# Optimization experiments

Hardware: AMD Instinct MI355X
Metric: run time of the kernel (lower is better)

The kernel has to match this reference:

```python
import jax, jax.numpy as jnp
import numpy as np

D_MODEL = 4096
N_HEADS = 32
N_KV_HEADS = 32
D_HEAD = 128
D_LATENT = 512
N_CKV = 4            # n_compressed_kv_heads = d_latent // d_head
T = 2048             # num_tokens (single-sequence prefill)
ROPE_BASE = 10000.0
NEG = -1e30


def _rope(x, positions):
    """Neox-style rotary embedding. x: (T, H, D)."""
    d = x.shape[-1]
    inv_freq = 1.0 / (ROPE_BASE ** (jnp.arange(0, d // 2, dtype=jnp.float32) * (2.0 / d)))
    freqs = positions.astype(jnp.float32)[:, None] * inv_freq[None, :]  # (T, D/2)
    cos = jnp.cos(freqs)[:, None, :]
    sin = jnp.sin(freqs)[:, None, :]
    x1, x2 = jnp.split(x, 2, axis=-1)
    return jnp.concatenate([x1 * cos - x2 * sin, x2 * cos + x1 * sin], axis=-1)


def setup_inputs() -> dict:
    key = jax.random.key(0)
    ks = jax.random.split(key, 6)
    s = jnp.float32(0.02)
    return {
        "positions": jnp.arange(T, dtype=jnp.int32),
        "hidden_states": jax.random.normal(ks[0], (T, D_MODEL), jnp.float32),
        "Wq": jax.random.normal(ks[1], (D_MODEL, N_HEADS * D_HEAD), jnp.float32) * s,
        "Wc": jax.random.normal(ks[2], (D_MODEL, 2 * D_LATENT), jnp.float32) * s,
        "Wuk": jax.random.normal(ks[3], (2 * D_LATENT, N_KV_HEADS * D_HEAD), jnp.float32) * s,
        "Wuv": jax.random.normal(ks[4], (2 * D_LATENT, N_KV_HEADS * D_HEAD), jnp.float32) * s,
        "Wo": jax.random.normal(ks[5], (N_HEADS * D_HEAD, D_MODEL), jnp.float32) * s,
    }


def reference(positions, hidden_states, Wq, Wc, Wuk, Wuv, Wo):
    # Q projection
    q = (hidden_states @ Wq).reshape(T, N_HEADS, D_HEAD)
    # MLA compression: hidden -> c_kv (2*d_latent), split into c_k / c_v
    c_kv = hidden_states @ Wc                                   # (T, 2*D_LATENT)
    c_k = c_kv[:, :D_LATENT].reshape(T, N_CKV, D_HEAD)          # compressed K cache
    c_v = c_kv[:, D_LATENT:].reshape(T, N_CKV, D_HEAD)          # compressed V cache
    # Decompression (computed by the source module; K is RoPE'd then discarded,
    # V is unused -- the v1 attention path runs over the compressed cache).
    K = (c_kv @ Wuk).reshape(T, N_KV_HEADS, D_HEAD)
    V = (c_kv @ Wuv).reshape(T, N_KV_HEADS, D_HEAD)             # noqa: unused, matches source
    # RoPE on q (and K, whose rotated value is dead in the source)
    q = _rope(q, positions)
    K = _rope(K, positions)  # dead, kept for FLOP parity with the source
    # GQA attention: n_heads=32 query heads over n_compressed_kv_heads=4 kv heads
    g = N_HEADS // N_CKV
    qg = q.reshape(T, N_CKV, g, D_HEAD)
    scale = jnp.float32(1.0 / np.sqrt(D_HEAD))
    scores = jnp.einsum('tkgd,skd->kgts', qg, c_k) * scale      # (N_CKV, g, T, T)
    causal = positions[:, None] >= positions[None, :]           # (T, T)
    scores = jnp.where(causal[None, None], scores, NEG)
    probs = jax.nn.softmax(scores, axis=-1)
    ctx = jnp.einsum('kgts,skd->tkgd', probs, c_v).reshape(T, N_HEADS * D_HEAD)
    return ctx @ Wo
```

## Files before the change

kernel.cpp:

```cpp
#include <hip/hip_runtime.h>
#include <hip/hip_bf16.h>
#include <cstdint>
#include <cstddef>


typedef unsigned short u16;
typedef short s16x8 __attribute__((ext_vector_type(8)));
typedef short s16x4 __attribute__((ext_vector_type(4)));
typedef float f32x4 __attribute__((ext_vector_type(4)));

#define MFMA16(a, b, c) __builtin_amdgcn_mfma_f32_16x16x32_bf16((a), (b), (c), 0, 0, 0)

#define QSCALE 0.12751899f
#define LOG2_ROPE_BASE 13.287712379549449f
#define FIXMAX 24.0f

__device__ __forceinline__ u16 f2b(float f) {
  return __builtin_bit_cast(u16, __float2bfloat16(f));
}
__device__ __forceinline__ void async_copy16(u16* lds, const u16* g) {
  __builtin_amdgcn_global_load_lds(
      (const __attribute__((address_space(1))) unsigned int*)g,
      (__attribute__((address_space(3))) unsigned int*)lds, 16, 0, 0);
}

__global__ __launch_bounds__(256)
void prep_kernel(const float* __restrict__ hidden, const float* __restrict__ Wq,
                 const float* __restrict__ Wc, const float* __restrict__ Wo,
                 u16* __restrict__ hb, u16* __restrict__ WqT,
                 u16* __restrict__ WcT, u16* __restrict__ WoT) {
  __shared__ alignas(16) u16 tile[64 * 72];
  const int b = blockIdx.x;
  const int t = threadIdx.x;

  if (b >= 9216) {
    int i = (b - 9216) * 256 + t;
    const float4* p = (const float4*)hidden + (size_t)i * 2;
    float4 a = p[0], c = p[1];
    s16x8 v;
    v[0] = (short)f2b(a.x); v[1] = (short)f2b(a.y);
    v[2] = (short)f2b(a.z); v[3] = (short)f2b(a.w);
    v[4] = (short)f2b(c.x); v[5] = (short)f2b(c.y);
    v[6] = (short)f2b(c.z); v[7] = (short)f2b(c.w);
    *(s16x8*)&hb[(size_t)i * 8] = v;
    return;
  }

  const float* in;
  u16* out;
  int gx, in_ld, out_ld;
  if (b < 4096)      { in = Wq; out = WqT; gx = b;        in_ld = 4096; out_ld = 4096; }
  else if (b < 5120) { in = Wc; out = WcT; gx = b - 4096; in_ld = 1024; out_ld = 4096; }
  else               { in = Wo; out = WoT; gx = b - 5120; in_ld = 4096; out_ld = 4096; }
  const int nbx = in_ld / 64;
  const int c0 = (gx % nbx) * 64, r0 = (gx / nbx) * 64;
  const int rr = t >> 3, cc = (t & 7) * 8;
#pragma unroll
  for (int p = 0; p < 2; p++) {
    int row = p * 32 + rr;
    const float4* src = (const float4*)&in[(size_t)(r0 + row) * in_ld + c0 + cc];
    float4 a = src[0], c = src[1];
    s16x8 v;
    v[0] = (short)f2b(a.x); v[1] = (short)f2b(a.y);
    v[2] = (short)f2b(a.z); v[3] = (short)f2b(a.w);
    v[4] = (short)f2b(c.x); v[5] = (short)f2b(c.y);
    v[6] = (short)f2b(c.z); v[7] = (short)f2b(c.w);
    *(s16x8*)&tile[row * 72 + cc] = v;
  }
  __syncthreads();
#pragma unroll
  for (int p = 0; p < 2; p++) {
    int orow = p * 32 + rr;
    s16x8 v;
#pragma unroll
    for (int j = 0; j < 8; j++) v[j] = (short)tile[(cc + j) * 72 + orow];
    *(s16x8*)&out[(size_t)(c0 + orow) * out_ld + r0 + cc] = v;
  }
}

__global__ __launch_bounds__(256)
void transpose_ckv(const u16* __restrict__ in, u16* __restrict__ out) {
  __shared__ alignas(16) u16 tile[64 * 72];
  const int kh = blockIdx.z;
  const int c0 = blockIdx.x * 64, r0 = blockIdx.y * 64;
  const int in_off = 512 + kh * 128;
  u16* outk = out + (size_t)kh * 128 * 2048;
  const int t = threadIdx.x;
  const int rr = t >> 3, cc = (t & 7) * 8;
#pragma unroll
  for (int p = 0; p < 2; p++) {
    int row = p * 32 + rr;
    s16x8 v = *(const s16x8*)&in[(size_t)(r0 + row) * 1024 + in_off + c0 + cc];
    *(s16x8*)&tile[row * 72 + cc] = v;
  }
  __syncthreads();
#pragma unroll
  for (int p = 0; p < 2; p++) {
    int orow = p * 32 + rr;
    s16x8 v;
#pragma unroll
    for (int j = 0; j < 8; j++) v[j] = (short)tile[(cc + j) * 72 + orow];
    *(s16x8*)&outk[(size_t)(c0 + orow) * 2048 + r0 + cc] = v;
  }
}

template <int EPI>
__global__ __launch_bounds__(256, 3)
void gemm_bt(const u16* __restrict__ A, const u16* __restrict__ Bt,
             void* __restrict__ Cv, void* __restrict__ Cv2,
             const int* __restrict__ positions) {
  __shared__ alignas(16) u16 As[2][128 * 32];
  __shared__ alignas(16) u16 Bs[2][128 * 32];

  const int tid = threadIdx.x;
  const int w = tid >> 6, l = tid & 63;
  const int wm = w >> 1, wn = w & 1;
  const int lrow = l >> 4, lcol = l & 15;
  const int m0 = blockIdx.y * 128, n0 = blockIdx.x * 128;

  f32x4 acc[4][4] = {};

  const int srow = l >> 2;
  const int scol = (l & 3) * 8;
  const u16* Ag = A + (size_t)(m0 + w * 32 + srow) * 4096 + scol;
  const u16* Bg = Bt + (size_t)(n0 + w * 32 + srow) * 4096 + scol;

  for (int kt = 0; kt < 4096; kt += 64) {
    __syncthreads();
#pragma unroll
    for (int hf = 0; hf < 2; hf++) {
      async_copy16(&As[hf][(w * 32) * 32], Ag + kt + hf * 32);
      async_copy16(&As[hf][(w * 32 + 16) * 32],
                   Ag + (size_t)16 * 4096 + kt + hf * 32);
      async_copy16(&Bs[hf][(w * 32) * 32], Bg + kt + hf * 32);
      async_copy16(&Bs[hf][(w * 32 + 16) * 32],
                   Bg + (size_t)16 * 4096 + kt + hf * 32);
    }
    __syncthreads();

#pragma unroll
    for (int hf = 0; hf < 2; hf++) {
      s16x8 a[4], b[4];
#pragma unroll
      for (int i = 0; i < 4; i++)
        a[i] = *(const s16x8*)&As[hf][(wm * 64 + i * 16 + lcol) * 32 + lrow * 8];
#pragma unroll
      for (int j = 0; j < 4; j++)
        b[j] = *(const s16x8*)&Bs[hf][(wn * 32 + (j & 1) * 16 + (j >> 1) * 64 +
                                       lcol) * 32 + lrow * 8];
#pragma unroll
      for (int i = 0; i < 4; i++)
#pragma unroll
        for (int j = 0; j < 4; j++)
          acc[i][j] = MFMA16(a[i], b[j], acc[i][j]);
    }
  }

  if constexpr (EPI == 3) {
    float* C = (float*)Cv;
#pragma unroll
    for (int i = 0; i < 4; i++) {
      int row = m0 + wm * 64 + i * 16 + lrow * 4;
#pragma unroll
      for (int j = 0; j < 4; j++) {
        int col = n0 + wn * 32 + (j & 1) * 16 + (j >> 1) * 64 + lcol;
#pragma unroll
        for (int r = 0; r < 4; r++)
          C[(size_t)(row + r) * 4096 + col] = acc[i][j][r];
      }
    }
  } else {
    if (n0 >= 4096) {
      u16* C = (u16*)Cv2;
      int cb = n0 - 4096;
#pragma unroll
      for (int i = 0; i < 4; i++) {
        int row = m0 + wm * 64 + i * 16 + lrow * 4;
#pragma unroll
        for (int j = 0; j < 4; j++) {
          int col = cb + wn * 32 + (j & 1) * 16 + (j >> 1) * 64 + lcol;
#pragma unroll
          for (int r = 0; r < 4; r++)
            C[(size_t)(row + r) * 1024 + col] = f2b(acc[i][j][r]);
        }
      }
    } else {
      u16* C = (u16*)Cv;
      float inv[2];
#pragma unroll
      for (int j = 0; j < 2; j++) {
        int d = wn * 32 + j * 16 + lcol;
        inv[j] = exp2f((float)d * (-LOG2_ROPE_BASE / 64.f));
      }
#pragma unroll
      for (int i = 0; i < 4; i++) {
        int row = m0 + wm * 64 + i * 16 + lrow * 4;
#pragma unroll
        for (int r = 0; r < 4; r++) {
          float pos = (float)positions[row + r];
#pragma unroll
          for (int j = 0; j < 2; j++) {
            int d = wn * 32 + j * 16 + lcol;
            float ang = pos * inv[j];
            float sv, cv;
            sincosf(ang, &sv, &cv);
            float x1 = acc[i][j][r];
            float x2 = acc[i][j + 2][r];
            C[(size_t)(row + r) * 4096 + n0 + d] = f2b((x1 * cv - x2 * sv) * QSCALE);
            C[(size_t)(row + r) * 4096 + n0 + d + 64] =
                f2b((x2 * cv + x1 * sv) * QSCALE);
          }
        }
      }
    }
  }
}

__global__ __launch_bounds__(256, 3)
void attn_kernel(const u16* __restrict__ Q, const u16* __restrict__ ckv,
                 const u16* __restrict__ vT, u16* __restrict__ ctx) {
  __shared__ alignas(16) u16 S0[16384];
  __shared__ alignas(16) u16 Ps[4][4096];
  __shared__ alignas(16) float red[4][32];

  const int tid = threadIdx.x, w = tid >> 6, l = tid & 63;
  const int lrow = l >> 4, lcol = l & 15;
  const int qt = (int)gridDim.x - 1 - (int)blockIdx.x;
  const int h = blockIdx.y, kh = h >> 3;
  const int q0w = w * 32;

  {
    const u16* qg = Q + (size_t)(qt * 128 + w * 32 + lrow) * 4096 + h * 128 + lcol * 8;
#pragma unroll
    for (int is = 0; is < 8; is++)
      async_copy16(&S0[(w * 32 + is * 4) * 128], qg + (size_t)is * 4 * 4096);
  }
  __syncthreads();
  s16x8 qf[2][4];
#pragma unroll
  for (int nt = 0; nt < 2; nt++)
#pragma unroll
    for (int kc = 0; kc < 4; kc++)
      qf[nt][kc] =
          *(const s16x8*)&S0[(q0w + nt * 16 + lcol) * 128 + kc * 32 + lrow * 8];

  u16* Kt = S0;
  u16* Vt = S0 + 8192;

  f32x4 o[2][8] = {};
  float l_run[2] = {0.f, 0.f};

  const int nkt = 2 * (qt + 1);
  for (int kt = 0; kt < nkt; kt++) {
    __syncthreads();
    {
      const u16* kg =
          ckv + (size_t)(kt * 64 + w * 16 + (l >> 2)) * 1024 + kh * 128 + (l & 3) * 8;
#pragma unroll
      for (int kc = 0; kc < 4; kc++)
        async_copy16(&Kt[kc * 2048 + (w * 16) * 32], kg + kc * 32);
      const u16* vg =
          vT + (size_t)(kh * 128 + w * 32 + (l >> 2)) * 2048 + kt * 64 + (l & 3) * 8;
#pragma unroll
      for (int kc = 0; kc < 2; kc++) {
        async_copy16(&Vt[kc * 4096 + (w * 32) * 32], vg + kc * 32);
        async_copy16(&Vt[kc * 4096 + (w * 32 + 16) * 32],
                     vg + (size_t)16 * 2048 + kc * 32);
      }
    }
    __syncthreads();

    f32x4 s[4][2] = {};
#pragma unroll
    for (int kc = 0; kc < 4; kc++)
#pragma unroll
      for (int mt = 0; mt < 4; mt++) {
        s16x8 ka = *(const s16x8*)&Kt[kc * 2048 + (mt * 16 + lcol) * 32 + lrow * 8];
        s[mt][0] = MFMA16(ka, qf[0][kc], s[mt][0]);
        s[mt][1] = MFMA16(ka, qf[1][kc], s[mt][1]);
      }

    if (kt >= 2 * qt) {
      int koff = (kt & 1) * 64;
#pragma unroll
      for (int mt = 0; mt < 4; mt++)
#pragma unroll
        for (int nt = 0; nt < 2; nt++)
#pragma unroll
          for (int r = 0; r < 4; r++) {
            int key = koff + mt * 16 + lrow * 4 + r;
            int q = q0w + nt * 16 + lcol;
            if (key > q) s[mt][nt][r] = -1e30f;
          }
    }

#pragma unroll
    for (int nt = 0; nt < 2; nt++) {
      float sum = 0.f;
#pragma unroll
      for (int mt = 0; mt < 4; mt++) {
        s16x4 pk;
#pragma unroll
        for (int r = 0; r < 4; r++) {
          float p = exp2f(s[mt][nt][r] - FIXMAX);
          sum += p;
          pk[r] = (short)f2b(p);
        }
        int key = mt * 16 + lrow * 4;
        *(s16x4*)&Ps[w][(key >> 5) * 2048 + (nt * 16 + lcol) * 32 + (key & 31)] = pk;
      }
      sum += __shfl_xor(sum, 16);
      sum += __shfl_xor(sum, 32);
      l_run[nt] += sum;
    }

#pragma unroll
    for (int kc = 0; kc < 2; kc++) {
      s16x8 pa0 = *(const s16x8*)&Ps[w][kc * 2048 + lcol * 32 + lrow * 8];
      s16x8 pa1 = *(const s16x8*)&Ps[w][kc * 2048 + (16 + lcol) * 32 + lrow * 8];
#pragma unroll
      for (int ntO = 0; ntO < 8; ntO++) {
        s16x8 vb = *(const s16x8*)&Vt[kc * 4096 + (ntO * 16 + lcol) * 32 + lrow * 8];
        o[0][ntO] = MFMA16(pa0, vb, o[0][ntO]);
        o[1][ntO] = MFMA16(pa1, vb, o[1][ntO]);
      }
    }
  }

  if (l < 16) {
    red[w][l] = 1.f / l_run[0];
    red[w][16 + l] = 1.f / l_run[1];
  }
  __syncthreads();
  f32x4 lf0 = *(const f32x4*)&red[w][lrow * 4];
  f32x4 lf1 = *(const f32x4*)&red[w][16 + lrow * 4];
#pragma unroll
  for (int mtO = 0; mtO < 2; mtO++)
#pragma unroll
    for (int ntO = 0; ntO < 8; ntO++)
#pragma unroll
      for (int r = 0; r < 4; r++) {
        float lv = mtO ? lf1[r] : lf0[r];
        int q = qt * 128 + q0w + mtO * 16 + lrow * 4 + r;
        int d = h * 128 + ntO * 16 + lcol;
        ctx[(size_t)q * 4096 + d] = f2b(o[mtO][ntO][r] * lv);
      }
}

extern "C" void kernel_launch(void* const* d_in, const int* in_sizes, int n_in,
                              void* d_out, int out_size, void* d_ws, size_t ws_size,
                              hipStream_t stream) {
  const int* positions = (const int*)d_in[0];
  const float* hidden = (const float*)d_in[1];
  const float* Wq = (const float*)d_in[2];
  const float* Wc = (const float*)d_in[3];
  const float* Wo = (const float*)d_in[6];

  char* ws = (char*)d_ws;
  u16* hb  = (u16*)(ws);
  u16* WT  = (u16*)(ws + 16777216);
  u16* qbf = (u16*)(ws + 58720256);
  u16* ckv = (u16*)(ws + 75497472);
  u16* cvT = (u16*)(ws + 79691776);
  u16* WoT = (u16*)(ws + 81788928);
  u16* ctx = hb;

  dim3 blk(256);

  prep_kernel<<<dim3(13312), blk, 0, stream>>>(hidden, Wq, Wc, Wo, hb, WT,
                                               WT + (size_t)4096 * 4096, WoT);

  gemm_bt<1><<<dim3(40, 16), blk, 0, stream>>>(hb, WT, qbf, ckv, positions);

  transpose_ckv<<<dim3(2, 32, 4), blk, 0, stream>>>(ckv, cvT);

  attn_kernel<<<dim3(16, 32), blk, 0, stream>>>(qbf, ckv, cvT, ctx);

  gemm_bt<3><<<dim3(32, 16), blk, 0, stream>>>(ctx, WoT, d_out, nullptr,
                                               positions);
}
```

Baseline: 507.9 us.

## Double-buffer K/V tiles, swizzle LDS, and pair causal query tiles per block

The attention kernel now double-buffers K and V tiles in LDS, prefetching the next tile while the current one is computed. It XOR-swizzles the LDS layouts of K, V and P to cut bank conflicts. Each block now handles two query tiles (qt and 15-qt), which balances the causal workload across a grid of 8x32 blocks. LDS use roughly doubles and the occupancy hint is dropped, so fewer blocks can be resident and there are fewer blocks overall.

New measurement: 482.8 us. -4.9%, faster.

```diff
diff --git a/kernel.cpp b/kernel.cpp
--- a/kernel.cpp
+++ b/kernel.cpp
@@ -216,135 +216,163 @@
   }
 }
 
-__global__ __launch_bounds__(256, 3)
+__global__ __launch_bounds__(256)
 void attn_kernel(const u16* __restrict__ Q, const u16* __restrict__ ckv,
                  const u16* __restrict__ vT, u16* __restrict__ ctx) {
-  __shared__ alignas(16) u16 S0[16384];
+  __shared__ alignas(16) u16 Kt[2][8192];
+  __shared__ alignas(16) u16 Vt[2][8192];
   __shared__ alignas(16) u16 Ps[4][4096];
   __shared__ alignas(16) float red[4][32];
 
   const int tid = threadIdx.x, w = tid >> 6, l = tid & 63;
   const int lrow = l >> 4, lcol = l & 15;
-  const int qt = (int)gridDim.x - 1 - (int)blockIdx.x;
   const int h = blockIdx.y, kh = h >> 3;
   const int q0w = w * 32;
-
-  {
-    const u16* qg = Q + (size_t)(qt * 128 + w * 32 + lrow) * 4096 + h * 128 + lcol * 8;
-#pragma unroll
-    for (int is = 0; is < 8; is++)
-      async_copy16(&S0[(w * 32 + is * 4) * 128], qg + (size_t)is * 4 * 4096);
-  }
-  __syncthreads();
-  s16x8 qf[2][4];
-#pragma unroll
-  for (int nt = 0; nt < 2; nt++)
-#pragma unroll
-    for (int kc = 0; kc < 4; kc++)
-      qf[nt][kc] =
-          *(const s16x8*)&S0[(q0w + nt * 16 + lcol) * 128 + kc * 32 + lrow * 8];
-
-  u16* Kt = S0;
-  u16* Vt = S0 + 8192;
-
-  f32x4 o[2][8] = {};
-  float l_run[2] = {0.f, 0.f};
-
-  const int nkt = 2 * (qt + 1);
-  for (int kt = 0; kt < nkt; kt++) {
+  const int sxor = (l >> 3) & 3;
+  const int kxor = (lcol >> 1) & 3;
+
+  const u16* kg0 = ckv + (size_t)(w * 16 + (l >> 2)) * 1024 + kh * 128 +
+                   (((l & 3) ^ sxor)) * 8;
+  const u16* vg0 = vT + (size_t)(kh * 128 + w * 32 + (l >> 2)) * 2048 +
+                   (((l & 3) ^ sxor)) * 8;
+
+#pragma unroll 1
+  for (int qi = 0; qi < 2; qi++) {
+    const int qt = qi ? (int)blockIdx.x : 15 - (int)blockIdx.x;
+
+    s16x8 qf[2][4];
+    {
+      const u16* qg =
+          Q + (size_t)(qt * 128 + q0w + lcol) * 4096 + h * 128 + lrow * 8;
+#pragma unroll
+      for (int nt = 0; nt < 2; nt++)
+#pragma unroll
+        for (int kc = 0; kc < 4; kc++)
+          qf[nt][kc] = *(const s16x8*)&qg[(size_t)(nt * 16) * 4096 + kc * 32];
+    }
+
+    f32x4 o[2][8] = {};
+    float l_run[2] = {0.f, 0.f};
+    const int nkt = 2 * (qt + 1);
+
+    {
+      const u16* kg = kg0;
+#pragma unroll
+      for (int kc = 0; kc < 4; kc++)
+        async_copy16(&Kt[0][kc * 2048 + (w * 16) * 32], kg + kc * 32);
+      const u16* vg = vg0;
+#pragma unroll
+      for (int kc = 0; kc < 2; kc++) {
+        async_copy16(&Vt[0][kc * 4096 + (w * 32) * 32], vg + kc * 32);
+        async_copy16(&Vt[0][kc * 4096 + (w * 32 + 16) * 32],
+                     vg + (size_t)16 * 2048 + kc * 32);
+      }
+    }
+    asm volatile("s_waitcnt vmcnt(0)" ::: "memory");
     __syncthreads();
-    {
-      const u16* kg =
-          ckv + (size_t)(kt * 64 + w * 16 + (l >> 2)) * 1024 + kh * 128 + (l & 3) * 8;
+
+#pragma unroll 1
+    for (int kt = 0; kt < nkt; kt++) {
+      const int cur = kt & 1;
+      if (kt + 1 < nkt) {
+        const u16* kg = kg0 + (size_t)(kt + 1) * 64 * 1024;
+#pragma unroll
+        for (int kc = 0; kc < 4; kc++)
+          async_copy16(&Kt[cur ^ 1][kc * 2048 + (w * 16) * 32], kg + kc * 32);
+        const u16* vg = vg0 + (size_t)(kt + 1) * 64;
+#pragma unroll
+        for (int kc = 0; kc < 2; kc++) {
+          async_copy16(&Vt[cur ^ 1][kc * 4096 + (w * 32) * 32], vg + kc * 32);
+          async_copy16(&Vt[cur ^ 1][kc * 4096 + (w * 32 + 16) * 32],
+                       vg + (size_t)16 * 2048 + kc * 32);
+        }
+      }
+
+      f32x4 s[4][2] = {};
 #pragma unroll
       for (int kc = 0; kc < 4; kc++)
-        async_copy16(&Kt[kc * 2048 + (w * 16) * 32], kg + kc * 32);
-      const u16* vg =
-          vT + (size_t)(kh * 128 + w * 32 + (l >> 2)) * 2048 + kt * 64 + (l & 3) * 8;
+#pragma unroll
+        for (int mt = 0; mt < 4; mt++) {
+          s16x8 ka = *(const s16x8*)&Kt[cur][kc * 2048 + (mt * 16 + lcol) * 32 +
+                                            (lrow ^ kxor) * 8];
+          s[mt][0] = MFMA16(ka, qf[0][kc], s[mt][0]);
+          s[mt][1] = MFMA16(ka, qf[1][kc], s[mt][1]);
+        }
+
+      if (kt >= 2 * qt) {
+        int koff = (kt & 1) * 64;
+#pragma unroll
+        for (int mt = 0; mt < 4; mt++)
+#pragma unroll
+          for (int nt = 0; nt < 2; nt++)
+#pragma unroll
+            for (int r = 0; r < 4; r++) {
+              int key = koff + mt * 16 + lrow * 4 + r;
+              int q = q0w + nt * 16 + lcol;
+              if (key > q) s[mt][nt][r] = -1e30f;
+            }
+      }
+
+#pragma unroll
+      for (int nt = 0; nt < 2; nt++) {
+        float sum = 0.f;
+#pragma unroll
+        for (int mt = 0; mt < 4; mt++) {
+          s16x4 pk;
+#pragma unroll
+          for (int r = 0; r < 4; r++) {
+            float p = exp2f(s[mt][nt][r] - FIXMAX);
+            sum += p;
+            pk[r] = (short)f2b(p);
+          }
+          int key = mt * 16 + lrow * 4;
+          *(s16x4*)&Ps[w][(key >> 5) * 2048 + (nt * 16 + lcol) * 32 +
+                          ((key & 31) ^ (kxor << 3))] = pk;
+        }
+        sum += __shfl_xor(sum, 16);
+        sum += __shfl_xor(sum, 32);
+        l_run[nt] += sum;
+      }
+
 #pragma unroll
       for (int kc = 0; kc < 2; kc++) {
-        async_copy16(&Vt[kc * 4096 + (w * 32) * 32], vg + kc * 32);
-        async_copy16(&Vt[kc * 4096 + (w * 32 + 16) * 32],
-                     vg + (size_t)16 * 2048 + kc * 32);
-      }
+        s16x8 pa0 = *(const s16x8*)&Ps[w][kc * 2048 + lcol * 32 +
+                                          (lrow ^ kxor) * 8];
+        s16x8 pa1 = *(const s16x8*)&Ps[w][kc * 2048 + (16 + lcol) * 32 +
+                                          (lrow ^ kxor) * 8];
+#pragma unroll
+        for (int ntO = 0; ntO < 8; ntO++) {
+          s16x8 vb = *(const s16x8*)&Vt[cur][kc * 4096 + (ntO * 16 + lcol) * 32 +
+                                             (lrow ^ kxor) * 8];
+          o[0][ntO] = MFMA16(pa0, vb, o[0][ntO]);
+          o[1][ntO] = MFMA16(pa1, vb, o[1][ntO]);
+        }
+      }
+
+      asm volatile("s_waitcnt vmcnt(0)" ::: "memory");
+      __syncthreads();
+    }
+
+    if (l < 16) {
+      red[w][l] = 1.f / l_run[0];
+      red[w][16 + l] = 1.f / l_run[1];
     }
     __syncthreads();
-
-    f32x4 s[4][2] = {};
-#pragma unroll
-    for (int kc = 0; kc < 4; kc++)
-#pragma unroll
-      for (int mt = 0; mt < 4; mt++) {
-        s16x8 ka = *(const s16x8*)&Kt[kc * 2048 + (mt * 16 + lcol) * 32 + lrow * 8];
-        s[mt][0] = MFMA16(ka, qf[0][kc], s[mt][0]);
-        s[mt][1] = MFMA16(ka, qf[1][kc], s[mt][1]);
-      }
-
-    if (kt >= 2 * qt) {
-      int koff = (kt & 1) * 64;
-#pragma unroll
-      for (int mt = 0; mt < 4; mt++)
-#pragma unroll
-        for (int nt = 0; nt < 2; nt++)
-#pragma unroll
-          for (int r = 0; r < 4; r++) {
-            int key = koff + mt * 16 + lrow * 4 + r;
-            int q = q0w + nt * 16 + lcol;
-            if (key > q) s[mt][nt][r] = -1e30f;
-          }
-    }
-
-#pragma unroll
-    for (int nt = 0; nt < 2; nt++) {
-      float sum = 0.f;
-#pragma unroll
-      for (int mt = 0; mt < 4; mt++) {
-        s16x4 pk;
+    f32x4 lf0 = *(const f32x4*)&red[w][lrow * 4];
+    f32x4 lf1 = *(const f32x4*)&red[w][16 + lrow * 4];
+#pragma unroll
+    for (int mtO = 0; mtO < 2; mtO++)
+#pragma unroll
+      for (int ntO = 0; ntO < 8; ntO++)
 #pragma unroll
         for (int r = 0; r < 4; r++) {
-          float p = exp2f(s[mt][nt][r] - FIXMAX);
-          sum += p;
-          pk[r] = (short)f2b(p);
-        }
-        int key = mt * 16 + lrow * 4;
-        *(s16x4*)&Ps[w][(key >> 5) * 2048 + (nt * 16 + lcol) * 32 + (key & 31)] = pk;
-      }
-      sum += __shfl_xor(sum, 16);
-      sum += __shfl_xor(sum, 32);
-      l_run[nt] += sum;
-    }
-
-#pragma unroll
-    for (int kc = 0; kc < 2; kc++) {
-      s16x8 pa0 = *(const s16x8*)&Ps[w][kc * 2048 + lcol * 32 + lrow * 8];
-      s16x8 pa1 = *(const s16x8*)&Ps[w][kc * 2048 + (16 + lcol) * 32 + lrow * 8];
-#pragma unroll
-      for (int ntO = 0; ntO < 8; ntO++) {
-        s16x8 vb = *(const s16x8*)&Vt[kc * 4096 + (ntO * 16 + lcol) * 32 + lrow * 8];
-        o[0][ntO] = MFMA16(pa0, vb, o[0][ntO]);
-        o[1][ntO] = MFMA16(pa1, vb, o[1][ntO]);
-      }
-    }
-  }
-
-  if (l < 16) {
-    red[w][l] = 1.f / l_run[0];
-    red[w][16 + l] = 1.f / l_run[1];
-  }
-  __syncthreads();
-  f32x4 lf0 = *(const f32x4*)&red[w][lrow * 4];
-  f32x4 lf1 = *(const f32x4*)&red[w][16 + lrow * 4];
-#pragma unroll
-  for (int mtO = 0; mtO < 2; mtO++)
-#pragma unroll
-    for (int ntO = 0; ntO < 8; ntO++)
-#pragma unroll
-      for (int r = 0; r < 4; r++) {
-        float lv = mtO ? lf1[r] : lf0[r];
-        int q = qt * 128 + q0w + mtO * 16 + lrow * 4 + r;
-        int d = h * 128 + ntO * 16 + lcol;
-        ctx[(size_t)q * 4096 + d] = f2b(o[mtO][ntO][r] * lv);
-      }
+          float lv = mtO ? lf1[r] : lf0[r];
+          int q = qt * 128 + q0w + mtO * 16 + lrow * 4 + r;
+          int d = h * 128 + ntO * 16 + lcol;
+          ctx[(size_t)q * 4096 + d] = f2b(o[mtO][ntO][r] * lv);
+        }
+    __syncthreads();
+  }
 }
 
 extern "C" void kernel_launch(void* const* d_in, const int* in_sizes, int n_in,
@@ -374,7 +402,7 @@
 
   transpose_ckv<<<dim3(2, 32, 4), blk, 0, stream>>>(ckv, cvT);
 
-  attn_kernel<<<dim3(16, 32), blk, 0, stream>>>(qbf, ckv, cvT, ctx);
+  attn_kernel<<<dim3(8, 32), blk, 0, stream>>>(qbf, ckv, cvT, ctx);
 
   gemm_bt<3><<<dim3(32, 16), blk, 0, stream>>>(ctx, WoT, d_out, nullptr,
                                                positions);
```
